# Performance work log

Measured on AMD Instinct MI355X. Metric: run time of the kernel, lower is better.

The kernel has to match this reference:

```python
import jax, jax.numpy as jnp
import numpy as np

TAU = 20.0   # membrane time constant (init default)
TH = 1.0     # spike threshold (init default)
K = 10.0     # surrogate sigmoid slope (hard-coded in forward)
EPS = 1e-6


def setup_inputs() -> dict:
    key = jax.random.key(0)
    I = jax.random.normal(key, (4096, 4096), dtype=jnp.float32)  # [B, L]
    return {"I": I}


def reference(I):
    B, L = I.shape

    def step(v, I_t):
        # Euler: dv = -v/tau + I ; v <- v + dv
        v = v - v / TAU + I_t
        s_soft = jax.nn.sigmoid(K * (v - TH))
        s_hard = (v >= TH).astype(I.dtype)
        # straight-through: value = s_hard, gradient flows through s_soft
        s = jax.lax.stop_gradient(s_hard - s_soft) + s_soft
        # reset: v <- v * (1 - stopgrad(s)); stopgrad(s) has value s_hard
        v = v * (1.0 - s_hard)
        return v, (s, s_hard)

    v0 = jnp.zeros((B,), dtype=I.dtype)
    _, (spikes_t, hard_t) = jax.lax.scan(step, v0, I.T)  # xs: [L, B]
    spikes = spikes_t.T       # [B, L]
    hard_spikes = hard_t.T    # [B, L]

    # hard latency: index of first hard spike, else L
    fired = hard_spikes > 0.5
    has = jnp.any(fired, axis=1)
    idx = jnp.argmax(fired, axis=1)
    hard_latency = jnp.where(has, idx, L).astype(jnp.int32)  # [B]

    # soft latency: spike-weighted mean time
    time = jnp.arange(L, dtype=spikes.dtype)
    w = spikes / (spikes.sum(axis=1, keepdims=True) + EPS)
    soft_latency = (w * time).sum(axis=1)  # [B]

    return spikes, hard_latency, soft_latency
```

## Files before the change

### kernel.cpp

```cpp
#include <hip/hip_runtime.h>

#define B_DIM 4096
#define L_DIM 4096
#define SEGLEN 256
#define NSEG (L_DIM / SEGLEN)
#define WARM 512
#define CHUNK 64
#define CF4 (CHUNK / 4)
#define LSTRIDE 68

__global__ __launch_bounds__(256) void init_kernel(float* wsf, int* wsi) {
    int i = blockIdx.x * 256 + threadIdx.x;
    if (i < 2 * B_DIM) wsf[i] = 0.f;
    if (i < B_DIM) wsi[i] = L_DIM;
}

#define LIF_CORE(IIN)                         \
    float q0 = u * cdiv;                      \
    float rr = fmaf(-20.0f, q0, u);           \
    float q  = fmaf(rr, cdiv, q0);            \
    float a  = u - q;                         \
    float b  = a + (IIN);                     \
    u = sp ? (IIN) : b;                       \
    sp = (u >= 1.0f);

#define WARM_STEP(IIN) { LIF_CORE(IIN) }

#define FULL_STEP(IIN, SOUT)                  \
    {                                         \
        LIF_CORE(IIN)                         \
        float sf = sp ? 1.0f : 0.0f;          \
        cnt += sf;                            \
        seen = fmaxf(seen, sf);               \
        accS += cnt;                          \
        accF += seen;                         \
        (SOUT) = sf;                          \
    }

__global__ __launch_bounds__(128, 1) void lif_kernel(const float* __restrict__ I,
                                                     float* __restrict__ out,
                                                     float* __restrict__ Cacc,
                                                     float* __restrict__ tsAcc,
                                                     int* __restrict__ firstAcc) {
    __shared__ __align__(16) float lds[2][64 * LSTRIDE];
    const int wid = threadIdx.x >> 6;
    const int lane = threadIdx.x & 63;
    const int seg = blockIdx.x >> 6;
    const int rowBase = (blockIdx.x & 63) * 64;
    const int t0 = seg * SEGLEN;
    const int start = (t0 > WARM) ? (t0 - WARM) : 0;
    const int nwarmCh = (t0 - start) / CHUNK;
    const int nch = nwarmCh + SEGLEN / CHUNK;

    if (wid == 1) {
        const int srow = lane >> 4, scol = lane & 15;
        const float* gb = I + (size_t)rowBase * L_DIM + start + scol * 4;
        {
            float* dst = &lds[0][0];
#pragma unroll
            for (int p = 0; p < 16; ++p) {
                const int r = 4 * p + srow;
                float4 v = *(const float4*)(gb + (size_t)r * L_DIM);
                *(float4*)&dst[r * LSTRIDE + scol * 4] = v;
            }
        }
        __syncthreads();
        for (int c = 0; c < nch; ++c) {
            if (c + 1 < nch) {
                const float* g = gb + (c + 1) * CHUNK;
                float* dst = &lds[(c + 1) & 1][0];
#pragma unroll
                for (int p = 0; p < 16; ++p) {
                    const int r = 4 * p + srow;
                    float4 v = *(const float4*)(g + (size_t)r * L_DIM);
                    *(float4*)&dst[r * LSTRIDE + scol * 4] = v;
                }
            }
            __syncthreads();
        }
    } else {
        const int row = rowBase + lane;
        float u = 0.f, cnt = 0.f, seen = 0.f, accS = 0.f, accF = 0.f;
        bool sp = false;
        const float cdiv = 0.05f;
        float* so = out + (size_t)row * L_DIM + t0;

        __syncthreads();
        for (int c = 0; c < nch; ++c) {
            const float* buf = &lds[c & 1][lane * LSTRIDE];
            float4 R[CF4];
#pragma unroll
            for (int j = 0; j < CF4; ++j) R[j] = *(const float4*)(buf + 4 * j);

            if (c < nwarmCh) {
#pragma unroll
                for (int j = 0; j < CF4; ++j) {
                    float4 iv = R[j];
                    WARM_STEP(iv.x) WARM_STEP(iv.y) WARM_STEP(iv.z) WARM_STEP(iv.w)
                }
            } else {
                float* sd = so + (c - nwarmCh) * CHUNK;
#pragma unroll
                for (int j = 0; j < CF4; ++j) {
                    float4 iv = R[j];
                    float4 sv;
                    FULL_STEP(iv.x, sv.x) FULL_STEP(iv.y, sv.y)
                    FULL_STEP(iv.z, sv.z) FULL_STEP(iv.w, sv.w)
                    *(float4*)(sd + 4 * j) = sv;
                }
            }
            __syncthreads();
        }

        if (cnt > 0.f) {
            const int firstLocal = (int)((float)SEGLEN - accF);
            atomicMin(&firstAcc[row], t0 + firstLocal);
        }
        atomicAdd(&Cacc[row], cnt);
        atomicAdd(&tsAcc[row], fmaf((float)(t0 + SEGLEN), cnt, -accS));
    }
}

__global__ __launch_bounds__(256) void fin_kernel(const float* __restrict__ Cacc,
                                                  const float* __restrict__ tsAcc,
                                                  const int* __restrict__ firstAcc,
                                                  float* __restrict__ out) {
    int r = blockIdx.x * 256 + threadIdx.x;
    if (r < B_DIM) {
        out[(size_t)B_DIM * L_DIM + r] = (float)firstAcc[r];
        out[(size_t)B_DIM * L_DIM + B_DIM + r] = tsAcc[r] / (Cacc[r] + 1e-6f);
    }
}

extern "C" void kernel_launch(void* const* d_in, const int* in_sizes, int n_in,
                              void* d_out, int out_size, void* d_ws, size_t ws_size,
                              hipStream_t stream) {
    const float* I = (const float*)d_in[0];
    float* out = (float*)d_out;
    float* wsf = (float*)d_ws;
    int* wsi = (int*)((float*)d_ws + 2 * B_DIM);
    (void)in_sizes; (void)n_in; (void)out_size; (void)ws_size;

    init_kernel<<<(2 * B_DIM + 255) / 256, 256, 0, stream>>>(wsf, wsi);
    lif_kernel<<<NSEG * 64, 128, 0, stream>>>(I, out, wsf, wsf + B_DIM, wsi);
    fin_kernel<<<(B_DIM + 255) / 256, 256, 0, stream>>>(wsf, wsf + B_DIM, wsi, out);
}
```

Baseline: 140.1 us.

## Replace producer-warp staging with direct global-to-LDS async loads and triple buffering

Removes the dedicated loader wavefront: each wave now computes its own segment and fetches input with global_load_lds into a swizzled triple buffer, using explicit vmcnt waits instead of block-wide barriers. Spike outputs are written back into LDS and transposed so global stores are row-coalesced, and block indices are remapped to group row blocks. The init kernel is replaced by memsets, with the first-spike sentinel clamped in the finalizer. The cost is hand-tuned vmcnt counts that must match exactly the number of outstanding loads, and the chunk size drops to 32.

```diff
diff --git a/kernel.cpp b/kernel.cpp
--- a/kernel.cpp
+++ b/kernel.cpp
@@ -5,15 +5,8 @@
 #define SEGLEN 256
 #define NSEG (L_DIM / SEGLEN)
 #define WARM 512
-#define CHUNK 64
-#define CF4 (CHUNK / 4)
-#define LSTRIDE 68
-
-__global__ __launch_bounds__(256) void init_kernel(float* wsf, int* wsi) {
-    int i = blockIdx.x * 256 + threadIdx.x;
-    if (i < 2 * B_DIM) wsf[i] = 0.f;
-    if (i < B_DIM) wsi[i] = L_DIM;
-}
+#define CHUNK 32
+#define LROW 32
 
 #define LIF_CORE(IIN)                         \
     float q0 = u * cdiv;                      \
@@ -37,88 +30,113 @@
         (SOUT) = sf;                          \
     }
 
+typedef const __attribute__((address_space(1))) void g_void;
+typedef __attribute__((address_space(3))) void l_void;
+__device__ __forceinline__ void gll16(const float* src, float* ldsbase) {
+    __builtin_amdgcn_global_load_lds((g_void*)src, (l_void*)ldsbase, 16, 0, 0);
+}
+
+#define VMCNT(N)                                             \
+    asm volatile("s_waitcnt vmcnt(" #N ")" ::: "memory");    \
+    __builtin_amdgcn_sched_barrier(0);
+
 __global__ __launch_bounds__(128, 1) void lif_kernel(const float* __restrict__ I,
                                                      float* __restrict__ out,
                                                      float* __restrict__ Cacc,
                                                      float* __restrict__ tsAcc,
                                                      int* __restrict__ firstAcc) {
-    __shared__ __align__(16) float lds[2][64 * LSTRIDE];
+    __shared__ __align__(16) float lds[2][3][64 * LROW];
     const int wid = threadIdx.x >> 6;
     const int lane = threadIdx.x & 63;
-    const int seg = blockIdx.x >> 6;
-    const int rowBase = (blockIdx.x & 63) * 64;
+    const int b = blockIdx.x;
+    const int rg = (b & 7) * 8 + ((b >> 3) & 7);
+    const int sp = b >> 6;
+    const int seg = 2 * sp + wid;
+    const int rowBase = rg * 64;
     const int t0 = seg * SEGLEN;
     const int start = (t0 > WARM) ? (t0 - WARM) : 0;
     const int nwarmCh = (t0 - start) / CHUNK;
     const int nch = nwarmCh + SEGLEN / CHUNK;
 
-    if (wid == 1) {
-        const int srow = lane >> 4, scol = lane & 15;
-        const float* gb = I + (size_t)rowBase * L_DIM + start + scol * 4;
-        {
-            float* dst = &lds[0][0];
-#pragma unroll
-            for (int p = 0; p < 16; ++p) {
-                const int r = 4 * p + srow;
-                float4 v = *(const float4*)(gb + (size_t)r * L_DIM);
-                *(float4*)&dst[r * LSTRIDE + scol * 4] = v;
-            }
-        }
-        __syncthreads();
-        for (int c = 0; c < nch; ++c) {
-            if (c + 1 < nch) {
-                const float* g = gb + (c + 1) * CHUNK;
-                float* dst = &lds[(c + 1) & 1][0];
-#pragma unroll
-                for (int p = 0; p < 16; ++p) {
-                    const int r = 4 * p + srow;
-                    float4 v = *(const float4*)(g + (size_t)r * L_DIM);
-                    *(float4*)&dst[r * LSTRIDE + scol * 4] = v;
-                }
-            }
-            __syncthreads();
-        }
-    } else {
-        const int row = rowBase + lane;
-        float u = 0.f, cnt = 0.f, seen = 0.f, accS = 0.f, accF = 0.f;
-        bool sp = false;
-        const float cdiv = 0.05f;
-        float* so = out + (size_t)row * L_DIM + t0;
+    const int srow = lane >> 3, scol = lane & 7;
+    const int swz = ((scol - srow) & 7) << 2;
+    const float* gbase = I + (size_t)rowBase * L_DIM + start;
 
-        __syncthreads();
-        for (int c = 0; c < nch; ++c) {
-            const float* buf = &lds[c & 1][lane * LSTRIDE];
-            float4 R[CF4];
-#pragma unroll
-            for (int j = 0; j < CF4; ++j) R[j] = *(const float4*)(buf + 4 * j);
+    float* bA = &lds[wid][0][0];
+    float* bB = &lds[wid][1][0];
+    float* bC = &lds[wid][2][0];
 
-            if (c < nwarmCh) {
-#pragma unroll
-                for (int j = 0; j < CF4; ++j) {
-                    float4 iv = R[j];
-                    WARM_STEP(iv.x) WARM_STEP(iv.y) WARM_STEP(iv.z) WARM_STEP(iv.w)
-                }
-            } else {
-                float* sd = so + (c - nwarmCh) * CHUNK;
-#pragma unroll
-                for (int j = 0; j < CF4; ++j) {
-                    float4 iv = R[j];
-                    float4 sv;
-                    FULL_STEP(iv.x, sv.x) FULL_STEP(iv.y, sv.y)
-                    FULL_STEP(iv.z, sv.z) FULL_STEP(iv.w, sv.w)
-                    *(float4*)(sd + 4 * j) = sv;
-                }
-            }
-            __syncthreads();
+    const int row = rowBase + lane;
+    float u = 0.f, cnt = 0.f, seen = 0.f, accS = 0.f, accF = 0.f;
+    bool sp_ = false;
+    const float cdiv = 0.05f;
+#define sp sp_
+
+#define GLL_CHUNK(CC, DST)                                              \
+    {                                                                   \
+        const float* gsrc = gbase + (size_t)(CC) * CHUNK;               \
+        _Pragma("unroll")                                               \
+        for (int p = 0; p < 8; ++p)                                     \
+            gll16(gsrc + (size_t)(8 * p + srow) * L_DIM + swz,          \
+                  (DST) + p * 256);                                     \
+    }
+
+    GLL_CHUNK(0, bA)
+    GLL_CHUNK(1, bB)
+
+    for (int c = 0; c < nch; ++c) {
+        if (c + 2 < nch) GLL_CHUNK(c + 2, bC)
+
+        if (c <= nwarmCh || c == nch - 1) {
+            VMCNT(16)
+        } else if (c == nwarmCh + 1 || c == nch - 2) {
+            VMCNT(24)
+        } else {
+            VMCNT(32)
         }
 
-        if (cnt > 0.f) {
-            const int firstLocal = (int)((float)SEGLEN - accF);
-            atomicMin(&firstAcc[row], t0 + firstLocal);
+        float4 R[8];
+#pragma unroll
+        for (int j = 0; j < 8; ++j)
+            R[j] = *(const float4*)&bA[lane * LROW + (((j + lane) & 7) << 2)];
+
+        if (c < nwarmCh) {
+#pragma unroll
+            for (int j = 0; j < 8; ++j) {
+                float4 iv = R[j];
+                WARM_STEP(iv.x) WARM_STEP(iv.y) WARM_STEP(iv.z) WARM_STEP(iv.w)
+            }
+        } else {
+#pragma unroll
+            for (int j = 0; j < 8; ++j) {
+                float4 iv = R[j];
+                float4 sv;
+                FULL_STEP(iv.x, sv.x) FULL_STEP(iv.y, sv.y)
+                FULL_STEP(iv.z, sv.z) FULL_STEP(iv.w, sv.w)
+                *(float4*)&bA[lane * LROW + (((j + lane) & 7) << 2)] = sv;
+            }
+            float4 S[8];
+#pragma unroll
+            for (int p = 0; p < 8; ++p)
+                S[p] = *(const float4*)&bA[p * 256 + (lane << 2)];
+            float* og = out + (size_t)rowBase * L_DIM + t0 +
+                        (size_t)(c - nwarmCh) * CHUNK;
+#pragma unroll
+            for (int p = 0; p < 8; ++p)
+                *(float4*)(og + (size_t)(8 * p + srow) * L_DIM + swz) = S[p];
         }
-        atomicAdd(&Cacc[row], cnt);
-        atomicAdd(&tsAcc[row], fmaf((float)(t0 + SEGLEN), cnt, -accS));
+
+        float* t = bA; bA = bB; bB = bC; bC = t;
     }
+
+    if (cnt > 0.f) {
+        const int firstLocal = (int)((float)SEGLEN - accF);
+        atomicMin(&firstAcc[row], t0 + firstLocal);
+    }
+    atomicAdd(&Cacc[row], cnt);
+    atomicAdd(&tsAcc[row], fmaf((float)(t0 + SEGLEN), cnt, -accS));
+#undef sp
+#undef GLL_CHUNK
 }
 
 __global__ __launch_bounds__(256) void fin_kernel(const float* __restrict__ Cacc,
@@ -127,7 +145,8 @@
                                                   float* __restrict__ out) {
     int r = blockIdx.x * 256 + threadIdx.x;
     if (r < B_DIM) {
-        out[(size_t)B_DIM * L_DIM + r] = (float)firstAcc[r];
+        int f = firstAcc[r];
+        out[(size_t)B_DIM * L_DIM + r] = (float)(f > L_DIM ? L_DIM : f);
         out[(size_t)B_DIM * L_DIM + B_DIM + r] = tsAcc[r] / (Cacc[r] + 1e-6f);
     }
 }
@@ -141,7 +160,8 @@
     int* wsi = (int*)((float*)d_ws + 2 * B_DIM);
     (void)in_sizes; (void)n_in; (void)out_size; (void)ws_size;
 
-    init_kernel<<<(2 * B_DIM + 255) / 256, 256, 0, stream>>>(wsf, wsi);
-    lif_kernel<<<NSEG * 64, 128, 0, stream>>>(I, out, wsf, wsf + B_DIM, wsi);
+    hipMemsetAsync(wsf, 0, 2 * B_DIM * sizeof(float), stream);
+    hipMemsetAsync(wsi, 0x7F, B_DIM * sizeof(int), stream);
+    lif_kernel<<<(B_DIM / 64) * (NSEG / 2), 128, 0, stream>>>(I, out, wsf, wsf + B_DIM, wsi);
     fin_kernel<<<(B_DIM + 255) / 256, 256, 0, stream>>>(wsf, wsf + B_DIM, wsi, out);
 }
```

Measured after the change: 146.5 us. 4.6% more time.
